# Performance work log

Hardware: AMD Instinct MI355X
Metric: run time of the kernel (lower is better)

## Reference

```python
import jax, jax.numpy as jnp
import numpy as np

EPS = 1e-8  # matches torch cosine_similarity eps


def setup_inputs() -> dict:
    key = jax.random.key(0)
    k1, k2 = jax.random.split(key)
    B, D = 8192, 128
    hid_positive = jax.random.normal(k1, (B, D), dtype=jnp.float32)
    hid_anchor = jax.random.normal(k2, (B, D), dtype=jnp.float32)
    return {"hid_positive": hid_positive, "hid_anchor": hid_anchor}


def reference(hid_positive, hid_anchor):
    # Original: anchor_batch = repeat_interleave(anchor, B) pairs every anchor i
    # with every positive j (positive[i] first per block, then the rest).
    # idx = +1 exactly on the (i, i) pairs, -1 elsewhere.
    # CosineEmbeddingLoss(margin=0, reduction='mean'):
    #   y=+1: 1 - cos ;  y=-1: max(0, cos)
    # Equivalent fused form: pairwise cosine matrix + masked loss, mean over B*B.
    a = hid_anchor / jnp.maximum(
        jnp.linalg.norm(hid_anchor, axis=1, keepdims=True), EPS)
    p = hid_positive / jnp.maximum(
        jnp.linalg.norm(hid_positive, axis=1, keepdims=True), EPS)
    cos = a @ p.T  # [B, B]; cos[i, j] = cos(anchor_i, positive_j)
    B = cos.shape[0]
    diag = jnp.eye(B, dtype=bool)
    loss = jnp.where(diag, 1.0 - cos, jnp.maximum(cos, 0.0))
    return jnp.mean(loss)
```

## Files before the change

kernel.cpp:

```cpp
#include <hip/hip_runtime.h>

typedef float f32x4 __attribute__((ext_vector_type(4)));
typedef int   i32x4 __attribute__((ext_vector_type(4)));
typedef int   i32x8 __attribute__((ext_vector_type(8)));

#define D 128

__global__ void normalize_diag_kernel(const float* __restrict__ anc,
                                      const float* __restrict__ pos,
                                      unsigned char* __restrict__ wsA,
                                      unsigned char* __restrict__ wsP,
                                      float* __restrict__ diagP,
                                      int* __restrict__ counter) {
  if (blockIdx.x == 0 && threadIdx.x == 0)
    __hip_atomic_store(counter, 0, __ATOMIC_RELAXED, __HIP_MEMORY_SCOPE_AGENT);
  __shared__ float rowc[16];
  const int t = threadIdx.x;
  const int rl = t >> 4, l16 = t & 15;
  const int row = blockIdx.x * 16 + rl;
  const float* ar = anc + (size_t)row * D + l16 * 8;
  const float* pr = pos + (size_t)row * D + l16 * 8;
  float4 a0 = *(const float4*)ar, a1 = *(const float4*)(ar + 4);
  float4 p0 = *(const float4*)pr, p1 = *(const float4*)(pr + 4);
  float av[8] = {a0.x, a0.y, a0.z, a0.w, a1.x, a1.y, a1.z, a1.w};
  float pv[8] = {p0.x, p0.y, p0.z, p0.w, p1.x, p1.y, p1.z, p1.w};
  float ssa = 0.f, ssp = 0.f;
#pragma unroll
  for (int k = 0; k < 8; ++k) { ssa += av[k] * av[k]; ssp += pv[k] * pv[k]; }
#pragma unroll
  for (int off = 1; off < 16; off <<= 1) {
    ssa += __shfl_xor(ssa, off);
    ssp += __shfl_xor(ssp, off);
  }
  const float sa = 1.f / fmaxf(sqrtf(ssa), 1e-8f);
  const float sp = 1.f / fmaxf(sqrtf(ssp), 1e-8f);
  float an[8], pn[8];
  float dot = 0.f;
#pragma unroll
  for (int k = 0; k < 8; ++k) {
    an[k] = av[k] * sa;
    pn[k] = pv[k] * sp;
    dot += an[k] * pn[k];
  }
  int wa0 = __builtin_amdgcn_cvt_pk_fp8_f32(an[0], an[1], 0, false);
  wa0 = __builtin_amdgcn_cvt_pk_fp8_f32(an[2], an[3], wa0, true);
  int wa1 = __builtin_amdgcn_cvt_pk_fp8_f32(an[4], an[5], 0, false);
  wa1 = __builtin_amdgcn_cvt_pk_fp8_f32(an[6], an[7], wa1, true);
  int wp0 = __builtin_amdgcn_cvt_pk_fp8_f32(pn[0], pn[1], 0, false);
  wp0 = __builtin_amdgcn_cvt_pk_fp8_f32(pn[2], pn[3], wp0, true);
  int wp1 = __builtin_amdgcn_cvt_pk_fp8_f32(pn[4], pn[5], 0, false);
  wp1 = __builtin_amdgcn_cvt_pk_fp8_f32(pn[6], pn[7], wp1, true);
  *(int2*)(wsA + (size_t)row * D + l16 * 8) = make_int2(wa0, wa1);
  *(int2*)(wsP + (size_t)row * D + l16 * 8) = make_int2(wp0, wp1);
#pragma unroll
  for (int off = 1; off < 16; off <<= 1) dot += __shfl_xor(dot, off);
  if (l16 == 0) rowc[rl] = 1.f - dot - fmaxf(dot, 0.f);
  __syncthreads();
  if (t == 0) {
    float s = 0.f;
#pragma unroll
    for (int i = 0; i < 16; ++i) s += rowc[i];
    diagP[blockIdx.x] = s;
  }
}

__global__ __launch_bounds__(512, 2) void gemm_relu_sum_kernel(
    const unsigned char* __restrict__ wsA,
    const unsigned char* __restrict__ wsP,
    float* __restrict__ partials, const float* __restrict__ diagP,
    int* __restrict__ counter, float* __restrict__ out, float invBB,
    int nBlocks) {
  __shared__ __align__(16) unsigned char ldsA[256 * 128];
  __shared__ __align__(16) unsigned char ldsB[2][128 * 128];
  __shared__ float wpart[8];
  __shared__ int lastFlag;
  const int tid = threadIdx.x;
  const int w = tid >> 6, l = tid & 63;
  const int r16 = l & 15, kg = l >> 4;
  const int wrow = w >> 2, wcol = w & 3;
  const int rp = blockIdx.x >> 3;
  const int cg = blockIdx.x & 7;

  const unsigned char* gA = wsA + (size_t)rp * 256 * D;

#pragma unroll
  for (int it = 0; it < 4; ++it) {
    const int g = it * 512 + tid;
    const int r = g >> 3, sl = g & 7;
    const int goff = r * 128 + ((sl ^ (r & 7)) * 16);
    const int lbase = (it * 512 + w * 64) * 16;
    __builtin_amdgcn_global_load_lds(
        (const __attribute__((address_space(1))) char*)(gA + goff),
        (__attribute__((address_space(3))) char*)((char*)ldsA + lbase), 16, 0, 0);
  }
  {
    const unsigned char* gBt = wsP + (size_t)(cg * 1024) * D;
#pragma unroll
    for (int it = 0; it < 2; ++it) {
      const int g = it * 512 + tid;
      const int r = g >> 3, sl = g & 7;
      const int goff = r * 128 + ((sl ^ (r & 7)) * 16);
      const int lbase = (it * 512 + w * 64) * 16;
      __builtin_amdgcn_global_load_lds(
          (const __attribute__((address_space(1))) char*)(gBt + goff),
          (__attribute__((address_space(3))) char*)((char*)ldsB[0] + lbase), 16, 0, 0);
    }
  }
  __syncthreads();

  i32x8 af[8];
#pragma unroll
  for (int m = 0; m < 8; ++m) {
    const int r = wrow * 128 + m * 16 + r16;
    const unsigned char* base = (const unsigned char*)ldsA + r * 128;
    i32x4 lo = *(const i32x4*)(base + (((2 * kg) ^ (r & 7)) * 16));
    i32x4 hi = *(const i32x4*)(base + (((2 * kg + 1) ^ (r & 7)) * 16));
    af[m] = __builtin_shufflevector(lo, hi, 0, 1, 2, 3, 4, 5, 6, 7);
  }

  float s = 0.f;
  for (int t = 0; t < 8; ++t) {
    if (t < 7) {
      const unsigned char* gBt = wsP + (size_t)(cg * 1024 + (t + 1) * 128) * D;
      char* lB = (char*)ldsB[(t + 1) & 1];
#pragma unroll
      for (int it = 0; it < 2; ++it) {
        const int g = it * 512 + tid;
        const int r = g >> 3, sl = g & 7;
        const int goff = r * 128 + ((sl ^ (r & 7)) * 16);
        const int lbase = (it * 512 + w * 64) * 16;
        __builtin_amdgcn_global_load_lds(
            (const __attribute__((address_space(1))) char*)(gBt + goff),
            (__attribute__((address_space(3))) char*)(lB + lbase), 16, 0, 0);
      }
    }

    const unsigned char* lB = (const unsigned char*)ldsB[t & 1];
    i32x8 bfr[2];
#pragma unroll
    for (int n = 0; n < 2; ++n) {
      const int r = wcol * 32 + n * 16 + r16;
      const unsigned char* base = lB + r * 128;
      i32x4 lo = *(const i32x4*)(base + (((2 * kg) ^ (r & 7)) * 16));
      i32x4 hi = *(const i32x4*)(base + (((2 * kg + 1) ^ (r & 7)) * 16));
      bfr[n] = __builtin_shufflevector(lo, hi, 0, 1, 2, 3, 4, 5, 6, 7);
    }

    f32x4 acc[8][2] = {};
    __builtin_amdgcn_s_setprio(1);
#pragma unroll
    for (int m = 0; m < 8; ++m)
#pragma unroll
      for (int n = 0; n < 2; ++n)
        acc[m][n] = __builtin_amdgcn_mfma_scale_f32_16x16x128_f8f6f4(
            af[m], bfr[n], acc[m][n], 0, 0,
            0, 0x7f7f7f7f, 0, 0x7f7f7f7f);
    __builtin_amdgcn_s_setprio(0);

#pragma unroll
    for (int m = 0; m < 8; ++m)
#pragma unroll
      for (int n = 0; n < 2; ++n)
#pragma unroll
        for (int q = 0; q < 4; ++q) s += fmaxf(acc[m][n][q], 0.f);

    __syncthreads();
  }

#pragma unroll
  for (int off = 32; off >= 1; off >>= 1) s += __shfl_xor(s, off);
  if (l == 0) wpart[w] = s;
  __syncthreads();
  if (tid == 0) {
    float b = 0.f;
#pragma unroll
    for (int i = 0; i < 8; ++i) b += wpart[i];
    __hip_atomic_store(&partials[blockIdx.x], b, __ATOMIC_RELAXED,
                       __HIP_MEMORY_SCOPE_AGENT);
    __threadfence();
    const int ticket = __hip_atomic_fetch_add(counter, 1, __ATOMIC_ACQ_REL,
                                              __HIP_MEMORY_SCOPE_AGENT);
    lastFlag = (ticket == nBlocks - 1) ? 1 : 0;
  }
  __syncthreads();

  if (lastFlag) {
    __threadfence();
    float v = diagP[tid];
    if (tid < nBlocks)
      v += __hip_atomic_load(&partials[tid], __ATOMIC_RELAXED,
                             __HIP_MEMORY_SCOPE_AGENT);
#pragma unroll
    for (int off = 32; off >= 1; off >>= 1) v += __shfl_xor(v, off);
    if (l == 0) wpart[w] = v;
    __syncthreads();
    if (tid == 0) {
      float tot = 0.f;
#pragma unroll
      for (int i = 0; i < 8; ++i) tot += wpart[i];
      out[0] = tot * invBB;
    }
  }
}

extern "C" void kernel_launch(void* const* d_in, const int* in_sizes, int n_in,
                              void* d_out, int out_size, void* d_ws, size_t ws_size,
                              hipStream_t stream) {
  const float* pos = (const float*)d_in[0];
  const float* anc = (const float*)d_in[1];
  const int B = in_sizes[0] / D;

  char* ws = (char*)d_ws;
  unsigned char* wsA = (unsigned char*)ws;
  unsigned char* wsP = (unsigned char*)(ws + (size_t)B * D);
  float* partials = (float*)(ws + (size_t)2 * B * D);
  float* diagP = partials + 256;
  int* counter = (int*)(diagP + 512);

  const int nDiag = B / 16;
  const int nBlocks = 256;
  const float invBB = 1.0f / ((float)B * (float)B);

  normalize_diag_kernel<<<nDiag, 256, 0, stream>>>(anc, pos, wsA, wsP, diagP,
                                                   counter);
  gemm_relu_sum_kernel<<<nBlocks, 512, 0, stream>>>(wsA, wsP, partials, diagP,
                                                    counter, (float*)d_out,
                                                    invBB, nBlocks);
}
```

Baseline: 30.23 us.

## Fuse normalization and GEMM into one kernel with a grid-wide barrier

```diff
diff --git a/kernel.cpp b/kernel.cpp
--- a/kernel.cpp
+++ b/kernel.cpp
@@ -5,84 +5,91 @@
 typedef int   i32x8 __attribute__((ext_vector_type(8)));
 
 #define D 128
-
-__global__ void normalize_diag_kernel(const float* __restrict__ anc,
-                                      const float* __restrict__ pos,
-                                      unsigned char* __restrict__ wsA,
-                                      unsigned char* __restrict__ wsP,
-                                      float* __restrict__ diagP,
-                                      int* __restrict__ counter) {
-  if (blockIdx.x == 0 && threadIdx.x == 0)
-    __hip_atomic_store(counter, 0, __ATOMIC_RELAXED, __HIP_MEMORY_SCOPE_AGENT);
-  __shared__ float rowc[16];
-  const int t = threadIdx.x;
-  const int rl = t >> 4, l16 = t & 15;
-  const int row = blockIdx.x * 16 + rl;
-  const float* ar = anc + (size_t)row * D + l16 * 8;
-  const float* pr = pos + (size_t)row * D + l16 * 8;
-  float4 a0 = *(const float4*)ar, a1 = *(const float4*)(ar + 4);
-  float4 p0 = *(const float4*)pr, p1 = *(const float4*)(pr + 4);
-  float av[8] = {a0.x, a0.y, a0.z, a0.w, a1.x, a1.y, a1.z, a1.w};
-  float pv[8] = {p0.x, p0.y, p0.z, p0.w, p1.x, p1.y, p1.z, p1.w};
-  float ssa = 0.f, ssp = 0.f;
-#pragma unroll
-  for (int k = 0; k < 8; ++k) { ssa += av[k] * av[k]; ssp += pv[k] * pv[k]; }
-#pragma unroll
-  for (int off = 1; off < 16; off <<= 1) {
-    ssa += __shfl_xor(ssa, off);
-    ssp += __shfl_xor(ssp, off);
-  }
-  const float sa = 1.f / fmaxf(sqrtf(ssa), 1e-8f);
-  const float sp = 1.f / fmaxf(sqrtf(ssp), 1e-8f);
-  float an[8], pn[8];
-  float dot = 0.f;
-#pragma unroll
-  for (int k = 0; k < 8; ++k) {
-    an[k] = av[k] * sa;
-    pn[k] = pv[k] * sp;
-    dot += an[k] * pn[k];
-  }
-  int wa0 = __builtin_amdgcn_cvt_pk_fp8_f32(an[0], an[1], 0, false);
-  wa0 = __builtin_amdgcn_cvt_pk_fp8_f32(an[2], an[3], wa0, true);
-  int wa1 = __builtin_amdgcn_cvt_pk_fp8_f32(an[4], an[5], 0, false);
-  wa1 = __builtin_amdgcn_cvt_pk_fp8_f32(an[6], an[7], wa1, true);
-  int wp0 = __builtin_amdgcn_cvt_pk_fp8_f32(pn[0], pn[1], 0, false);
-  wp0 = __builtin_amdgcn_cvt_pk_fp8_f32(pn[2], pn[3], wp0, true);
-  int wp1 = __builtin_amdgcn_cvt_pk_fp8_f32(pn[4], pn[5], 0, false);
-  wp1 = __builtin_amdgcn_cvt_pk_fp8_f32(pn[6], pn[7], wp1, true);
-  *(int2*)(wsA + (size_t)row * D + l16 * 8) = make_int2(wa0, wa1);
-  *(int2*)(wsP + (size_t)row * D + l16 * 8) = make_int2(wp0, wp1);
-#pragma unroll
-  for (int off = 1; off < 16; off <<= 1) dot += __shfl_xor(dot, off);
-  if (l16 == 0) rowc[rl] = 1.f - dot - fmaxf(dot, 0.f);
-  __syncthreads();
-  if (t == 0) {
-    float s = 0.f;
-#pragma unroll
-    for (int i = 0; i < 16; ++i) s += rowc[i];
-    diagP[blockIdx.x] = s;
-  }
-}
-
-__global__ __launch_bounds__(512, 2) void gemm_relu_sum_kernel(
-    const unsigned char* __restrict__ wsA,
-    const unsigned char* __restrict__ wsP,
-    float* __restrict__ partials, const float* __restrict__ diagP,
-    int* __restrict__ counter, float* __restrict__ out, float invBB,
-    int nBlocks) {
+#define NBLK 256
+
+__global__ __launch_bounds__(512, 2) void fused_loss_kernel(
+    const float* __restrict__ anc, const float* __restrict__ pos,
+    unsigned char* __restrict__ wsA, unsigned char* __restrict__ wsP,
+    float* __restrict__ partials, float* __restrict__ diagP,
+    int* __restrict__ c0, int* __restrict__ c1,
+    float* __restrict__ out, float invBB) {
   __shared__ __align__(16) unsigned char ldsA[256 * 128];
   __shared__ __align__(16) unsigned char ldsB[2][128 * 128];
   __shared__ float wpart[8];
   __shared__ int lastFlag;
   const int tid = threadIdx.x;
+  const int bid = blockIdx.x;
   const int w = tid >> 6, l = tid & 63;
+
+  {
+    const int rl = tid >> 4, l16 = tid & 15;
+    const int row = bid * 32 + rl;
+    const float* ar = anc + (size_t)row * D + l16 * 8;
+    const float* pr = pos + (size_t)row * D + l16 * 8;
+    float4 a0 = *(const float4*)ar, a1 = *(const float4*)(ar + 4);
+    float4 p0 = *(const float4*)pr, p1 = *(const float4*)(pr + 4);
+    float av[8] = {a0.x, a0.y, a0.z, a0.w, a1.x, a1.y, a1.z, a1.w};
+    float pv[8] = {p0.x, p0.y, p0.z, p0.w, p1.x, p1.y, p1.z, p1.w};
+    float ssa = 0.f, ssp = 0.f;
+#pragma unroll
+    for (int k = 0; k < 8; ++k) { ssa += av[k] * av[k]; ssp += pv[k] * pv[k]; }
+#pragma unroll
+    for (int off = 1; off < 16; off <<= 1) {
+      ssa += __shfl_xor(ssa, off);
+      ssp += __shfl_xor(ssp, off);
+    }
+    const float sa = 1.f / fmaxf(sqrtf(ssa), 1e-8f);
+    const float sp = 1.f / fmaxf(sqrtf(ssp), 1e-8f);
+    float an[8], pn[8];
+    float dot = 0.f;
+#pragma unroll
+    for (int k = 0; k < 8; ++k) {
+      an[k] = av[k] * sa;
+      pn[k] = pv[k] * sp;
+      dot += an[k] * pn[k];
+    }
+    int wa0 = __builtin_amdgcn_cvt_pk_fp8_f32(an[0], an[1], 0, false);
+    wa0 = __builtin_amdgcn_cvt_pk_fp8_f32(an[2], an[3], wa0, true);
+    int wa1 = __builtin_amdgcn_cvt_pk_fp8_f32(an[4], an[5], 0, false);
+    wa1 = __builtin_amdgcn_cvt_pk_fp8_f32(an[6], an[7], wa1, true);
+    int wp0 = __builtin_amdgcn_cvt_pk_fp8_f32(pn[0], pn[1], 0, false);
+    wp0 = __builtin_amdgcn_cvt_pk_fp8_f32(pn[2], pn[3], wp0, true);
+    int wp1 = __builtin_amdgcn_cvt_pk_fp8_f32(pn[4], pn[5], 0, false);
+    wp1 = __builtin_amdgcn_cvt_pk_fp8_f32(pn[6], pn[7], wp1, true);
+    *(int2*)(wsA + (size_t)row * D + l16 * 8) = make_int2(wa0, wa1);
+    *(int2*)(wsP + (size_t)row * D + l16 * 8) = make_int2(wp0, wp1);
+#pragma unroll
+    for (int off = 1; off < 16; off <<= 1) dot += __shfl_xor(dot, off);
+    float c = (l16 == 0) ? (1.f - dot - fmaxf(dot, 0.f)) : 0.f;
+#pragma unroll
+    for (int off = 1; off < 64; off <<= 1) c += __shfl_xor(c, off);
+    if (l == 0) wpart[w] = c;
+    __syncthreads();
+    if (tid == 0) {
+      float sD = 0.f;
+#pragma unroll
+      for (int i = 0; i < 8; ++i) sD += wpart[i];
+      diagP[bid] = sD;
+    }
+  }
+
+  __threadfence();
+  __syncthreads();
+  if (tid == 0) {
+    __hip_atomic_fetch_add(c0, 1, __ATOMIC_RELEASE, __HIP_MEMORY_SCOPE_AGENT);
+    while (__hip_atomic_load(c0, __ATOMIC_RELAXED, __HIP_MEMORY_SCOPE_AGENT) <
+           NBLK)
+      __builtin_amdgcn_s_sleep(2);
+  }
+  __syncthreads();
+  __threadfence();
+
   const int r16 = l & 15, kg = l >> 4;
   const int wrow = w >> 2, wcol = w & 3;
-  const int rp = blockIdx.x >> 3;
-  const int cg = blockIdx.x & 7;
+  const int rp = bid >> 3;
+  const int cg = bid & 7;
 
   const unsigned char* gA = wsA + (size_t)rp * 256 * D;
-
 #pragma unroll
   for (int it = 0; it < 4; ++it) {
     const int g = it * 512 + tid;
@@ -118,7 +125,7 @@
     af[m] = __builtin_shufflevector(lo, hi, 0, 1, 2, 3, 4, 5, 6, 7);
   }
 
-  float s = 0.f;
+  float s0 = 0.f, s1 = 0.f, s2 = 0.f, s3 = 0.f;
   for (int t = 0; t < 8; ++t) {
     if (t < 7) {
       const unsigned char* gBt = wsP + (size_t)(cg * 1024 + (t + 1) * 128) * D;
@@ -160,13 +167,17 @@
 #pragma unroll
     for (int m = 0; m < 8; ++m)
 #pragma unroll
-      for (int n = 0; n < 2; ++n)
-#pragma unroll
-        for (int q = 0; q < 4; ++q) s += fmaxf(acc[m][n][q], 0.f);
+      for (int n = 0; n < 2; ++n) {
+        s0 += fmaxf(acc[m][n][0], 0.f);
+        s1 += fmaxf(acc[m][n][1], 0.f);
+        s2 += fmaxf(acc[m][n][2], 0.f);
+        s3 += fmaxf(acc[m][n][3], 0.f);
+      }
 
     __syncthreads();
   }
 
+  float s = (s0 + s1) + (s2 + s3);
 #pragma unroll
   for (int off = 32; off >= 1; off >>= 1) s += __shfl_xor(s, off);
   if (l == 0) wpart[w] = s;
@@ -175,21 +186,22 @@
     float b = 0.f;
 #pragma unroll
     for (int i = 0; i < 8; ++i) b += wpart[i];
-    __hip_atomic_store(&partials[blockIdx.x], b, __ATOMIC_RELAXED,
+    __hip_atomic_store(&partials[bid], b, __ATOMIC_RELAXED,
                        __HIP_MEMORY_SCOPE_AGENT);
     __threadfence();
-    const int ticket = __hip_atomic_fetch_add(counter, 1, __ATOMIC_ACQ_REL,
+    const int ticket = __hip_atomic_fetch_add(c1, 1, __ATOMIC_ACQ_REL,
                                               __HIP_MEMORY_SCOPE_AGENT);
-    lastFlag = (ticket == nBlocks - 1) ? 1 : 0;
+    lastFlag = (ticket == NBLK - 1) ? 1 : 0;
   }
   __syncthreads();
 
   if (lastFlag) {
     __threadfence();
-    float v = diagP[tid];
-    if (tid < nBlocks)
-      v += __hip_atomic_load(&partials[tid], __ATOMIC_RELAXED,
-                             __HIP_MEMORY_SCOPE_AGENT);
+    float v = 0.f;
+    if (tid < NBLK)
+      v = __hip_atomic_load(&partials[tid], __ATOMIC_RELAXED,
+                            __HIP_MEMORY_SCOPE_AGENT) +
+          diagP[tid];
 #pragma unroll
     for (int off = 32; off >= 1; off >>= 1) v += __shfl_xor(v, off);
     if (l == 0) wpart[w] = v;
@@ -214,16 +226,13 @@
   unsigned char* wsA = (unsigned char*)ws;
   unsigned char* wsP = (unsigned char*)(ws + (size_t)B * D);
   float* partials = (float*)(ws + (size_t)2 * B * D);
-  float* diagP = partials + 256;
-  int* counter = (int*)(diagP + 512);
-
-  const int nDiag = B / 16;
-  const int nBlocks = 256;
+  float* diagP = partials + NBLK;
+  int* counters = (int*)(diagP + NBLK);
+
   const float invBB = 1.0f / ((float)B * (float)B);
 
-  normalize_diag_kernel<<<nDiag, 256, 0, stream>>>(anc, pos, wsA, wsP, diagP,
-                                                   counter);
-  gemm_relu_sum_kernel<<<nBlocks, 512, 0, stream>>>(wsA, wsP, partials, diagP,
-                                                    counter, (float*)d_out,
-                                                    invBB, nBlocks);
+  hipMemsetAsync(counters, 0, 8, stream);
+  fused_loss_kernel<<<NBLK, 512, 0, stream>>>(anc, pos, wsA, wsP, partials,
+                                              diagP, counters, counters + 1,
+                                              (float*)d_out, invBB);
 }
```

Result: slower. 110.3 us (+265.0%).

## Deepen B-tile prefetch to four LDS buffers with vmcnt-based waits

Applied to the files above, without the earlier changes.

```diff
diff --git a/kernel.cpp b/kernel.cpp
--- a/kernel.cpp
+++ b/kernel.cpp
@@ -5,6 +5,7 @@
 typedef int   i32x8 __attribute__((ext_vector_type(8)));
 
 #define D 128
+#define NBLK 256
 
 __global__ void normalize_diag_kernel(const float* __restrict__ anc,
                                       const float* __restrict__ pos,
@@ -68,20 +69,36 @@
     const unsigned char* __restrict__ wsA,
     const unsigned char* __restrict__ wsP,
     float* __restrict__ partials, const float* __restrict__ diagP,
-    int* __restrict__ counter, float* __restrict__ out, float invBB,
-    int nBlocks) {
+    int* __restrict__ counter, float* __restrict__ out, float invBB) {
   __shared__ __align__(16) unsigned char ldsA[256 * 128];
-  __shared__ __align__(16) unsigned char ldsB[2][128 * 128];
+  __shared__ __align__(16) unsigned char ldsB[4][128 * 128];
   __shared__ float wpart[8];
   __shared__ int lastFlag;
   const int tid = threadIdx.x;
+  const int bid = blockIdx.x;
   const int w = tid >> 6, l = tid & 63;
   const int r16 = l & 15, kg = l >> 4;
   const int wrow = w >> 2, wcol = w & 3;
-  const int rp = blockIdx.x >> 3;
-  const int cg = blockIdx.x & 7;
+  const int rp = bid >> 3;
+  const int cg = bid & 7;
 
   const unsigned char* gA = wsA + (size_t)rp * 256 * D;
+  const unsigned char* gB = wsP + (size_t)(cg * 1024) * D;
+
+#define STAGE_B(buf, tile)                                                     \
+  {                                                                            \
+    const unsigned char* gBt = gB + (size_t)(tile) * 128 * D;                  \
+    char* lB = (char*)ldsB[buf];                                               \
+    _Pragma("unroll") for (int it = 0; it < 2; ++it) {                         \
+      const int g = it * 512 + tid;                                            \
+      const int r = g >> 3, sl = g & 7;                                        \
+      const int goff = r * 128 + ((sl ^ (r & 7)) * 16);                        \
+      const int lbase = (it * 512 + w * 64) * 16;                              \
+      __builtin_amdgcn_global_load_lds(                                        \
+          (const __attribute__((address_space(1))) char*)(gBt + goff),         \
+          (__attribute__((address_space(3))) char*)(lB + lbase), 16, 0, 0);    \
+    }                                                                          \
+  }
 
 #pragma unroll
   for (int it = 0; it < 4; ++it) {
@@ -93,20 +110,11 @@
         (const __attribute__((address_space(1))) char*)(gA + goff),
         (__attribute__((address_space(3))) char*)((char*)ldsA + lbase), 16, 0, 0);
   }
-  {
-    const unsigned char* gBt = wsP + (size_t)(cg * 1024) * D;
-#pragma unroll
-    for (int it = 0; it < 2; ++it) {
-      const int g = it * 512 + tid;
-      const int r = g >> 3, sl = g & 7;
-      const int goff = r * 128 + ((sl ^ (r & 7)) * 16);
-      const int lbase = (it * 512 + w * 64) * 16;
-      __builtin_amdgcn_global_load_lds(
-          (const __attribute__((address_space(1))) char*)(gBt + goff),
-          (__attribute__((address_space(3))) char*)((char*)ldsB[0] + lbase), 16, 0, 0);
-    }
-  }
-  __syncthreads();
+  STAGE_B(0, 0)
+  STAGE_B(1, 1)
+
+  asm volatile("s_waitcnt vmcnt(4)" ::: "memory");
+  __builtin_amdgcn_s_barrier();
 
   i32x8 af[8];
 #pragma unroll
@@ -118,24 +126,16 @@
     af[m] = __builtin_shufflevector(lo, hi, 0, 1, 2, 3, 4, 5, 6, 7);
   }
 
-  float s = 0.f;
+  float s0 = 0.f, s1 = 0.f, s2 = 0.f, s3 = 0.f;
+#pragma unroll
   for (int t = 0; t < 8; ++t) {
-    if (t < 7) {
-      const unsigned char* gBt = wsP + (size_t)(cg * 1024 + (t + 1) * 128) * D;
-      char* lB = (char*)ldsB[(t + 1) & 1];
-#pragma unroll
-      for (int it = 0; it < 2; ++it) {
-        const int g = it * 512 + tid;
-        const int r = g >> 3, sl = g & 7;
-        const int goff = r * 128 + ((sl ^ (r & 7)) * 16);
-        const int lbase = (it * 512 + w * 64) * 16;
-        __builtin_amdgcn_global_load_lds(
-            (const __attribute__((address_space(1))) char*)(gBt + goff),
-            (__attribute__((address_space(3))) char*)(lB + lbase), 16, 0, 0);
-      }
-    }
-
-    const unsigned char* lB = (const unsigned char*)ldsB[t & 1];
+    if (t < 6) STAGE_B((t + 2) & 3, t + 2)
+    if (t < 6)      asm volatile("s_waitcnt vmcnt(4)" ::: "memory");
+    else if (t == 6) asm volatile("s_waitcnt vmcnt(2)" ::: "memory");
+    else             asm volatile("s_waitcnt vmcnt(0)" ::: "memory");
+    __builtin_amdgcn_s_barrier();
+
+    const unsigned char* lB = (const unsigned char*)ldsB[t & 3];
     i32x8 bfr[2];
 #pragma unroll
     for (int n = 0; n < 2; ++n) {
@@ -160,13 +160,15 @@
 #pragma unroll
     for (int m = 0; m < 8; ++m)
 #pragma unroll
-      for (int n = 0; n < 2; ++n)
-#pragma unroll
-        for (int q = 0; q < 4; ++q) s += fmaxf(acc[m][n][q], 0.f);
-
-    __syncthreads();
-  }
-
+      for (int n = 0; n < 2; ++n) {
+        s0 += fmaxf(acc[m][n][0], 0.f);
+        s1 += fmaxf(acc[m][n][1], 0.f);
+        s2 += fmaxf(acc[m][n][2], 0.f);
+        s3 += fmaxf(acc[m][n][3], 0.f);
+      }
+  }
+
+  float s = (s0 + s1) + (s2 + s3);
 #pragma unroll
   for (int off = 32; off >= 1; off >>= 1) s += __shfl_xor(s, off);
   if (l == 0) wpart[w] = s;
@@ -175,19 +177,19 @@
     float b = 0.f;
 #pragma unroll
     for (int i = 0; i < 8; ++i) b += wpart[i];
-    __hip_atomic_store(&partials[blockIdx.x], b, __ATOMIC_RELAXED,
+    __hip_atomic_store(&partials[bid], b, __ATOMIC_RELAXED,
                        __HIP_MEMORY_SCOPE_AGENT);
     __threadfence();
     const int ticket = __hip_atomic_fetch_add(counter, 1, __ATOMIC_ACQ_REL,
                                               __HIP_MEMORY_SCOPE_AGENT);
-    lastFlag = (ticket == nBlocks - 1) ? 1 : 0;
+    lastFlag = (ticket == NBLK - 1) ? 1 : 0;
   }
   __syncthreads();
 
   if (lastFlag) {
     __threadfence();
     float v = diagP[tid];
-    if (tid < nBlocks)
+    if (tid < NBLK)
       v += __hip_atomic_load(&partials[tid], __ATOMIC_RELAXED,
                              __HIP_MEMORY_SCOPE_AGENT);
 #pragma unroll
@@ -201,6 +203,7 @@
       out[0] = tot * invBB;
     }
   }
+#undef STAGE_B
 }
 
 extern "C" void kernel_launch(void* const* d_in, const int* in_sizes, int n_in,
@@ -214,16 +217,14 @@
   unsigned char* wsA = (unsigned char*)ws;
   unsigned char* wsP = (unsigned char*)(ws + (size_t)B * D);
   float* partials = (float*)(ws + (size_t)2 * B * D);
-  float* diagP = partials + 256;
+  float* diagP = partials + NBLK;
   int* counter = (int*)(diagP + 512);
 
   const int nDiag = B / 16;
-  const int nBlocks = 256;
   const float invBB = 1.0f / ((float)B * (float)B);
 
   normalize_diag_kernel<<<nDiag, 256, 0, stream>>>(anc, pos, wsA, wsP, diagP,
                                                    counter);
-  gemm_relu_sum_kernel<<<nBlocks, 512, 0, stream>>>(wsA, wsP, partials, diagP,
-                                                    counter, (float*)d_out,
-                                                    invBB, nBlocks);
+  gemm_relu_sum_kernel<<<NBLK, 512, 0, stream>>>(wsA, wsP, partials, diagP,
+                                                 counter, (float*)d_out, invBB);
 }
```

After: 31.39 us. 1.04x slower.
